# Kernel optimization log

Measured on AMD Instinct MI355X. Metric: run time of the kernel, lower is better.

## Reference

```python
import jax, jax.numpy as jnp
import numpy as np

B, C, H, W = 8, 384, 32, 32
NUM_HEADS = 8
HEAD_DIM = C // NUM_HEADS


def setup_inputs() -> dict:
    key = jax.random.key(0)
    k1, k2, k3, k4, k5 = jax.random.split(key, 5)
    s = 1.0 / np.sqrt(C)
    return {
        "x": jax.random.normal(k1, (B, C, H, W), dtype=jnp.float32),
        "w_qkv": jax.random.normal(k2, (3 * C, C), dtype=jnp.float32) * s,   # 1x1 conv == linear over channels
        "b_qkv": jax.random.normal(k3, (3 * C,), dtype=jnp.float32) * 0.01,
        "w_proj": jax.random.normal(k4, (C, C), dtype=jnp.float32) * s,
        "b_proj": jax.random.normal(k5, (C,), dtype=jnp.float32) * 0.01,
    }


def reference(x, w_qkv, b_qkv, w_proj, b_proj):
    b, c, h, w = x.shape
    n = h * w
    scale = HEAD_DIM ** (-0.5)
    # 1x1 conv qkv: (B, 3C, H, W)
    qkv = jnp.einsum('bchw,oc->bohw', x, w_qkv) + b_qkv[None, :, None, None]
    # 'b (three hd d) h0 w0 -> three b hd (h0 w0) d'
    qkv = qkv.reshape(b, 3, NUM_HEADS, HEAD_DIM, n)
    qkv = jnp.transpose(qkv, (1, 0, 2, 4, 3))  # (3, B, heads, N, d)
    q, k, v = qkv[0], qkv[1], qkv[2]
    attn = jnp.einsum('bhnd,bhmd->bhnm', q, k) * scale
    attn = jax.nn.softmax(attn, axis=-1)
    out = jnp.einsum('bhnm,bhmd->bhnd', attn, v)          # (B, heads, N, d)
    out = jnp.transpose(out, (0, 1, 3, 2)).reshape(b, c, h, w)  # b (hd d) h w
    out = jnp.einsum('bchw,oc->bohw', out, w_proj) + b_proj[None, :, None, None]
    return out
```

## Files before the change

kernel.cpp:

```cpp
#include <hip/hip_runtime.h>
#include <hip/hip_bf16.h>

typedef __hip_bfloat16 bf16;
typedef __bf16 bfx8 __attribute__((ext_vector_type(8)));
typedef float f32x4 __attribute__((ext_vector_type(4)));

#define Bk   8
#define Ck   384
#define NHk  8
#define Dk   48
#define Dp   64
#define Nk   1024
#define O3   1152


__device__ __forceinline__ void gload_lds16(const bf16* src, void* dst)
{
    __builtin_amdgcn_global_load_lds(
        (const __attribute__((address_space(1))) void*)src,
        (__attribute__((address_space(3))) void*)dst, 16, 0, 0);
}

__global__ __launch_bounds__(256) void prep_kernel(
    const float* __restrict__ x, bf16* __restrict__ Xs,
    const float* __restrict__ wq, const float* __restrict__ wp,
    bf16* __restrict__ Wq, bf16* __restrict__ Wp,
    bf16* __restrict__ Qs, bf16* __restrict__ Ks)
{
    __shared__ bf16 tile[32][33];
    if (blockIdx.x < 3072) {
        const int id = blockIdx.x;
        const int b = id / 384, rem = id % 384;
        const int c0 = ((rem >> 5) % 12) * 32, n0 = (rem & 31) * 32;
        const int tn = threadIdx.x & 31, tc = threadIdx.x >> 5;
        const float* xb = x + (size_t)b * Ck * Nk;
        #pragma unroll
        for (int i = 0; i < 4; ++i)
            tile[tc + 8 * i][tn] = __float2bfloat16(xb[(size_t)(c0 + tc + 8 * i) * Nk + n0 + tn]);
        __syncthreads();
        bf16* base = Xs + ((size_t)b * 64 + (n0 >> 4)) * 48 * 128 + (c0 >> 3) * 128;
        #pragma unroll
        for (int i = 0; i < 4; ++i) {
            int n_loc = tc + 8 * i, c_loc = tn;
            base[(size_t)(n_loc >> 4) * 6144 + (c_loc >> 3) * 128 +
                 (n_loc & 15) * 8 + (c_loc & 7)] = tile[c_loc][n_loc];
        }
    } else {
        int i = (blockIdx.x - 3072) * 256 + threadIdx.x;
        if (i < O3 * Ck) {
            int o = i / Ck, c = i - o * Ck;
            Wq[((size_t)(o >> 4) * 48 + (c >> 3)) * 128 + (o & 15) * 8 + (c & 7)] =
                __float2bfloat16(wq[i]);
        }
        if (i < Ck * Ck) {
            int o = i / Ck, c = i - o * Ck;
            Wp[((size_t)(o >> 4) * 48 + (c >> 3)) * 128 + (o & 15) * 8 + (c & 7)] =
                __float2bfloat16(wp[i]);
        }
        if (i < 262144) {
            int buf = i >> 17;
            int r17 = i & 131071;
            int head = r17 >> 11;
            int r11 = r17 & 2047;
            int g = r11 >> 5, c5 = r11 & 31;
            int cd = 6 + (c5 >> 4), e = c5 & 15;
            bf16* p = (buf ? Ks : Qs) + (size_t)head * 65536 +
                      ((size_t)g * 8 + cd) * 128 + e * 8;
            *(int4*)p = (int4){0, 0, 0, 0};
        }
    }
}

__global__ __launch_bounds__(256) void qkv_mfma_kernel(
    const bf16* __restrict__ Xs, const bf16* __restrict__ Wq,
    const float* __restrict__ bias,
    bf16* __restrict__ Qs, bf16* __restrict__ Ks, bf16* __restrict__ Vs)
{
    __shared__ __align__(16) bf16 Wl[24576];

    const int b    = blockIdx.z;
    const int by   = blockIdx.y;
    const int bx   = blockIdx.x;
    const int o0   = by * 64;
    const int n0   = bx * 128;
    const int wave = threadIdx.x >> 6;
    const int lane = threadIdx.x & 63;
    const int l15  = lane & 15, quad = lane >> 4;
    const int t3   = o0 / Ck;

    {
        const bf16* wsrc = Wq + (size_t)by * 24576;
        #pragma unroll
        for (int i = 0; i < 12; ++i) {
            int f = wave * 12 + i;
            gload_lds16(wsrc + f * 512 + lane * 8, (char*)Wl + f * 1024);
        }
    }

    const bf16* xg[2];
    #pragma unroll
    for (int i = 0; i < 2; ++i)
        xg[i] = Xs + ((size_t)(b * 64 + bx * 8 + wave * 2 + i) * 48) * 128 + lane * 8;
    const bf16* wl = Wl + lane * 8;

    f32x4 acc[8];
    #pragma unroll
    for (int i = 0; i < 8; ++i) acc[i] = (f32x4){0.f, 0.f, 0.f, 0.f};

    asm volatile("s_waitcnt vmcnt(0)" ::: "memory");
    __syncthreads();

    if (t3 < 2) {
        #pragma unroll
        for (int s = 0; s < 12; ++s) {
            bfx8 fx[2], fw[4];
            #pragma unroll
            for (int i = 0; i < 2; ++i) fx[i] = *(const bfx8*)(xg[i] + s * 512);
            #pragma unroll
            for (int j = 0; j < 4; ++j) fw[j] = *(const bfx8*)(wl + j * 6144 + s * 512);
            #pragma unroll
            for (int i = 0; i < 2; ++i)
                #pragma unroll
                for (int j = 0; j < 4; ++j)
                    acc[i * 4 + j] = __builtin_amdgcn_mfma_f32_16x16x32_bf16(
                        fx[i], fw[j], acc[i * 4 + j], 0, 0, 0);
        }
        const float qscale = 0.2082350964f;
        #pragma unroll
        for (int j = 0; j < 4; ++j) {
            int o  = o0 + j * 16 + l15;
            float bi = bias[o];
            int r  = o - t3 * Ck;
            int hd = r / Dk, d = r - hd * Dk;
            bf16* hb = (t3 == 0 ? Qs : Ks) + (size_t)(b * NHk + hd) * 65536
                     + (d >> 3) * 128 + (d & 7);
            #pragma unroll
            for (int i = 0; i < 2; ++i) {
                #pragma unroll
                for (int reg = 0; reg < 4; ++reg) {
                    int npos = n0 + wave * 32 + i * 16 + quad * 4 + reg;
                    float v = acc[i * 4 + j][reg] + bi;
                    if (t3 == 0) v *= qscale;
                    hb[(size_t)(npos >> 4) * 1024 + (npos & 15) * 8] = __float2bfloat16(v);
                }
            }
        }
    } else {
        #pragma unroll
        for (int s = 0; s < 12; ++s) {
            bfx8 fx[2], fw[4];
            #pragma unroll
            for (int i = 0; i < 2; ++i) fx[i] = *(const bfx8*)(xg[i] + s * 512);
            #pragma unroll
            for (int j = 0; j < 4; ++j) fw[j] = *(const bfx8*)(wl + j * 6144 + s * 512);
            #pragma unroll
            for (int j = 0; j < 4; ++j)
                #pragma unroll
                for (int i = 0; i < 2; ++i)
                    acc[j * 2 + i] = __builtin_amdgcn_mfma_f32_16x16x32_bf16(
                        fw[j], fx[i], acc[j * 2 + i], 0, 0, 0);
        }
        #pragma unroll
        for (int j = 0; j < 4; ++j) {
            #pragma unroll
            for (int reg = 0; reg < 4; ++reg) {
                int o  = o0 + j * 16 + quad * 4 + reg;
                float bi = bias[o];
                int r  = o - 2 * Ck;
                int hd = r / Dk, d = r - hd * Dk;
                bf16* vb = Vs + (size_t)(b * NHk + hd) * 49152
                         + ((size_t)(d >> 4) * 128) * 128 + (d & 15) * 8;
                #pragma unroll
                for (int i = 0; i < 2; ++i) {
                    int npos = n0 + wave * 32 + i * 16 + l15;
                    vb[(size_t)(npos >> 3) * 128 + (npos & 7)] =
                        __float2bfloat16(acc[j * 2 + i][reg] + bi);
                }
            }
        }
    }
}

__global__ __launch_bounds__(256, 2) void attn_kernel(
    const bf16* __restrict__ Qs, const bf16* __restrict__ Ks,
    const bf16* __restrict__ Vs, bf16* __restrict__ AO)
{
    __shared__ __align__(16) bf16 KbL[2][4096];
    __shared__ __align__(16) bf16 VbL[2][3072];
    __shared__ __align__(16) short Ps[4 * 2 * 1152];
    __shared__ float sums[4][2][16];

    const int hd   = blockIdx.x;
    const int b    = blockIdx.y;
    const int bx   = blockIdx.z;
    const int t    = threadIdx.x;
    const int wave = t >> 6;
    const int lane = t & 63;
    const int l15  = lane & 15;
    const int quad = lane >> 4;
    const int grp16 = (bx * 4 + wave) * 2;

    const bf16* qb = Qs + (size_t)(b * NHk + hd) * 65536;
    const bf16* kb = Ks + (size_t)(b * NHk + hd) * 65536;
    const bf16* vb = Vs + (size_t)(b * NHk + hd) * 49152;

    auto stage = [&](int buf, int k0) {
        const bf16* ksrc = kb + (size_t)k0 * 64;
        const bf16* vsrc = vb + (size_t)(k0 >> 3) * 128;
        char* kdst = (char*)&KbL[buf][0];
        char* vdst = (char*)&VbL[buf][0];
        #pragma unroll
        for (int i = 0; i < 4; ++i) {
            const int l = wave + i * 4;
            if (l < 14) {
                const int piece = l >> 1, half = l & 1;
                const bf16* src; char* dst;
                if (piece < 4) {
                    src = ksrc + piece * 1024 + half * 512 + lane * 8;
                    dst = kdst + piece * 2048 + half * 1024;
                } else {
                    const int dc = piece - 4;
                    src = vsrc + (size_t)dc * 16384 + half * 512 + lane * 8;
                    dst = vdst + dc * 2048 + half * 1024;
                }
                gload_lds16(src, dst);
            }
        }
    };

    stage(0, 0);

    bfx8 bq[2][2];
    #pragma unroll
    for (int qt = 0; qt < 2; ++qt) {
        const bf16* qp = qb + ((size_t)(grp16 + qt) * 8 + quad) * 128 + l15 * 8;
        bq[qt][0] = *(const bfx8*)(qp);
        bq[qt][1] = *(const bfx8*)(qp + 512);
    }

    float l_run[2] = {0.f, 0.f};
    f32x4 oacc[2][3];
    #pragma unroll
    for (int qt = 0; qt < 2; ++qt)
        #pragma unroll
        for (int dc = 0; dc < 3; ++dc) oacc[qt][dc] = (f32x4){0.f, 0.f, 0.f, 0.f};

    short* const PsW[2] = { Ps + wave * 2304, Ps + wave * 2304 + 1152 };
    const int lo = quad * 128 + l15 * 8;

    asm volatile("s_waitcnt vmcnt(0)" ::: "memory");
    __syncthreads();

    auto step = [&](int buf, int k0, bool pf) {
        if (pf) stage(buf ^ 1, k0 + 64);

        const bf16* Kc = &KbL[buf][0];
        const bf16* Vc = &VbL[buf][0];

        f32x4 sf[2][4];
        #pragma unroll
        for (int s = 0; s < 4; ++s) {
            const bfx8 kf0 = *(const bfx8*)(Kc + s * 1024 + lo);
            const bfx8 kf1 = *(const bfx8*)(Kc + s * 1024 + 512 + lo);
            #pragma unroll
            for (int qt = 0; qt < 2; ++qt) {
                f32x4 z = (f32x4){0.f, 0.f, 0.f, 0.f};
                z = __builtin_amdgcn_mfma_f32_16x16x32_bf16(kf0, bq[qt][0], z, 0, 0, 0);
                z = __builtin_amdgcn_mfma_f32_16x16x32_bf16(kf1, bq[qt][1], z, 0, 0, 0);
                sf[qt][s] = z;
            }
        }

        #pragma unroll
        for (int qt = 0; qt < 2; ++qt) {
            float lsum = 0.f;
            #pragma unroll
            for (int s = 0; s < 4; ++s) {
                ushort4 pk;
                float e0 = __builtin_amdgcn_exp2f(sf[qt][s][0]);
                float e1 = __builtin_amdgcn_exp2f(sf[qt][s][1]);
                float e2 = __builtin_amdgcn_exp2f(sf[qt][s][2]);
                float e3 = __builtin_amdgcn_exp2f(sf[qt][s][3]);
                lsum += (e0 + e1) + (e2 + e3);
                bf16 h0 = __float2bfloat16(e0), h1 = __float2bfloat16(e1);
                bf16 h2 = __float2bfloat16(e2), h3 = __float2bfloat16(e3);
                pk.x = *(unsigned short*)&h0; pk.y = *(unsigned short*)&h1;
                pk.z = *(unsigned short*)&h2; pk.w = *(unsigned short*)&h3;
                *(ushort4*)&PsW[qt][l15 * 72 + s * 16 + quad * 4] = pk;
            }
            l_run[qt] += lsum;
        }

        #pragma unroll
        for (int qt = 0; qt < 2; ++qt) {
            const bfx8 ap0 = *(const bfx8*)&PsW[qt][l15 * 72 + quad * 8];
            const bfx8 ap1 = *(const bfx8*)&PsW[qt][l15 * 72 + 32 + quad * 8];
            #pragma unroll
            for (int dc = 0; dc < 3; ++dc) {
                const bfx8 bv0 = *(const bfx8*)(Vc + dc * 1024 + lo);
                const bfx8 bv1 = *(const bfx8*)(Vc + dc * 1024 + 512 + lo);
                oacc[qt][dc] = __builtin_amdgcn_mfma_f32_16x16x32_bf16(
                    ap0, bv0, oacc[qt][dc], 0, 0, 0);
                oacc[qt][dc] = __builtin_amdgcn_mfma_f32_16x16x32_bf16(
                    ap1, bv1, oacc[qt][dc], 0, 0, 0);
            }
        }

        asm volatile("s_waitcnt vmcnt(0)" ::: "memory");
        __syncthreads();
    };

    #pragma unroll 1
    for (int k0 = 0; k0 < Nk; k0 += 128) {
        step(0, k0, true);
        step(1, k0 + 64, k0 + 128 < Nk);
    }

    #pragma unroll
    for (int qt = 0; qt < 2; ++qt) {
        float lt = l_run[qt];
        lt += __shfl_xor(lt, 16, 64);
        lt += __shfl_xor(lt, 32, 64);
        sums[wave][qt][l15] = lt;
    }

    #pragma unroll
    for (int qt = 0; qt < 2; ++qt) {
        short* OsW = PsW[qt];
        #pragma unroll
        for (int r = 0; r < 4; ++r) {
            int qi = quad * 4 + r;
            float rli = 1.0f / sums[wave][qt][qi];
            #pragma unroll
            for (int dcc = 0; dcc < 3; ++dcc) {
                bf16 hb = __float2bfloat16(oacc[qt][dcc][r] * rli);
                OsW[qi * 64 + dcc * 16 + l15] = *(short*)&hb;
            }
        }
    }

    #pragma unroll
    for (int qt = 0; qt < 2; ++qt) {
        bf16* aob = AO + (((size_t)b * 64 + grp16 + qt) * 48 + hd * 6) * 128;
        short* OsW = PsW[qt];
        int u = lane;
        int4 v = *(const int4*)&OsW[(u & 15) * 64 + (u >> 4) * 8];
        *(int4*)(aob + u * 8) = v;
        if (lane < 32) {
            int u2 = 64 + lane;
            int4 v2 = *(const int4*)&OsW[(u2 & 15) * 64 + (u2 >> 4) * 8];
            *(int4*)(aob + u2 * 8) = v2;
        }
    }
}

__global__ __launch_bounds__(256) void proj_mfma_kernel(
    const bf16* __restrict__ AO, const bf16* __restrict__ Wp,
    const float* __restrict__ bias, float* __restrict__ out)
{
    __shared__ __align__(16) bf16 Wl[24576];

    const int b    = blockIdx.z;
    const int by   = blockIdx.y;
    const int bx   = blockIdx.x;
    const int o0   = by * 64;
    const int n0   = bx * 128;
    const int wave = threadIdx.x >> 6;
    const int lane = threadIdx.x & 63;
    const int l15  = lane & 15, quad = lane >> 4;

    {
        const bf16* wsrc = Wp + (size_t)by * 24576;
        #pragma unroll
        for (int i = 0; i < 12; ++i) {
            int f = wave * 12 + i;
            gload_lds16(wsrc + f * 512 + lane * 8, (char*)Wl + f * 1024);
        }
    }

    const bf16* ag[2];
    #pragma unroll
    for (int i = 0; i < 2; ++i)
        ag[i] = AO + ((size_t)(b * 64 + bx * 8 + wave * 2 + i) * 48) * 128 + lane * 8;
    const bf16* wl = Wl + lane * 8;

    f32x4 acc[8];
    #pragma unroll
    for (int i = 0; i < 8; ++i) acc[i] = (f32x4){0.f, 0.f, 0.f, 0.f};

    asm volatile("s_waitcnt vmcnt(0)" ::: "memory");
    __syncthreads();

    #pragma unroll
    for (int s = 0; s < 12; ++s) {
        bfx8 fx[2], fw[4];
        #pragma unroll
        for (int i = 0; i < 2; ++i) fx[i] = *(const bfx8*)(ag[i] + s * 512);
        #pragma unroll
        for (int j = 0; j < 4; ++j) fw[j] = *(const bfx8*)(wl + j * 6144 + s * 512);
        #pragma unroll
        for (int j = 0; j < 4; ++j)
            #pragma unroll
            for (int i = 0; i < 2; ++i)
                acc[j * 2 + i] = __builtin_amdgcn_mfma_f32_16x16x32_bf16(
                    fw[j], fx[i], acc[j * 2 + i], 0, 0, 0);
    }

    #pragma unroll
    for (int j = 0; j < 4; ++j) {
        #pragma unroll
        for (int reg = 0; reg < 4; ++reg) {
            int o  = o0 + j * 16 + quad * 4 + reg;
            float bi = bias[o];
            #pragma unroll
            for (int i = 0; i < 2; ++i) {
                int npos = n0 + wave * 32 + i * 16 + l15;
                out[((size_t)b * Ck + o) * Nk + npos] = acc[j * 2 + i][reg] + bi;
            }
        }
    }
}

extern "C" void kernel_launch(void* const* d_in, const int* in_sizes, int n_in,
                              void* d_out, int out_size, void* d_ws, size_t ws_size,
                              hipStream_t stream)
{
    const float* x      = (const float*)d_in[0];
    const float* w_qkv  = (const float*)d_in[1];
    const float* b_qkv  = (const float*)d_in[2];
    const float* w_proj = (const float*)d_in[3];
    const float* b_proj = (const float*)d_in[4];
    float* out = (float*)d_out;

    const size_t XT_SEG = (size_t)Bk * Nk * Ck;
    const size_t WQ_SEG = (size_t)O3 * Ck;
    const size_t WP_SEG = (size_t)Ck * Ck;
    const size_t QK_SEG = (size_t)Bk * NHk * Nk * Dp;
    const size_t V_SEG  = (size_t)Bk * NHk * Dk * Nk;

    bf16* Xs = (bf16*)d_ws;
    bf16* Wq = Xs + XT_SEG;
    bf16* Wp = Wq + WQ_SEG;
    bf16* Qs = Wp + WP_SEG;
    bf16* Ks = Qs + QK_SEG;
    bf16* Vs = Ks + QK_SEG;
    bf16* AO = Vs + V_SEG;

    prep_kernel<<<3072 + (O3 * Ck + 255) / 256, 256, 0, stream>>>(
        x, Xs, w_qkv, w_proj, Wq, Wp, Qs, Ks);
    qkv_mfma_kernel<<<dim3(Nk / 128, O3 / 64, Bk), 256, 0, stream>>>(
        Xs, Wq, b_qkv, Qs, Ks, Vs);
    attn_kernel<<<dim3(NHk, Bk, 8), 256, 0, stream>>>(Qs, Ks, Vs, AO);
    proj_mfma_kernel<<<dim3(Nk / 128, Ck / 64, Bk), 256, 0, stream>>>(
        AO, Wp, b_proj, out);
}
```

Before: 120.5 us.

## Vectorize prep conversion and GEMM epilogue stores via operand swaps

The prep kernel no longer uses an LDS tile transpose. Each thread now reads 8 channel values for one position and writes a packed 16-byte bf16 chunk, and the weight conversion is packed the same way. In the QKV and projection GEMMs the MFMA operand order is swapped so each lane's accumulator registers run along the contiguous output dimension, which lets the epilogue emit 8-byte bf16 or 16-byte float stores in place of scalar ones. The attention kernel also gains explicit lgkmcnt waits and reuses a shared pack helper. The channel reads in prep are strided by N per element, so coalescing now relies on adjacent threads reading adjacent positions.

```diff
diff --git a/kernel.cpp b/kernel.cpp
--- a/kernel.cpp
+++ b/kernel.cpp
@@ -21,53 +21,68 @@
         (__attribute__((address_space(3))) void*)dst, 16, 0, 0);
 }
 
+__device__ __forceinline__ int pack2(float a, float b)
+{
+    bf16 ha = __float2bfloat16(a), hb = __float2bfloat16(b);
+    unsigned lo = *(unsigned short*)&ha, hi = *(unsigned short*)&hb;
+    return (int)(lo | (hi << 16));
+}
+
+__device__ __forceinline__ ushort4 pack4(float v0, float v1, float v2, float v3)
+{
+    bf16 h0 = __float2bfloat16(v0), h1 = __float2bfloat16(v1);
+    bf16 h2 = __float2bfloat16(v2), h3 = __float2bfloat16(v3);
+    ushort4 pk;
+    pk.x = *(unsigned short*)&h0; pk.y = *(unsigned short*)&h1;
+    pk.z = *(unsigned short*)&h2; pk.w = *(unsigned short*)&h3;
+    return pk;
+}
+
 __global__ __launch_bounds__(256) void prep_kernel(
     const float* __restrict__ x, bf16* __restrict__ Xs,
     const float* __restrict__ wq, const float* __restrict__ wp,
     bf16* __restrict__ Wq, bf16* __restrict__ Wp,
     bf16* __restrict__ Qs, bf16* __restrict__ Ks)
 {
-    __shared__ bf16 tile[32][33];
-    if (blockIdx.x < 3072) {
-        const int id = blockIdx.x;
-        const int b = id / 384, rem = id % 384;
-        const int c0 = ((rem >> 5) % 12) * 32, n0 = (rem & 31) * 32;
-        const int tn = threadIdx.x & 31, tc = threadIdx.x >> 5;
+    const int u = blockIdx.x * 256 + threadIdx.x;
+    if (u < 393216) {
+        int n = u & 1023, rest = u >> 10;
+        int oct = rest % 48, b = rest / 48;
         const float* xb = x + (size_t)b * Ck * Nk;
-        #pragma unroll
-        for (int i = 0; i < 4; ++i)
-            tile[tc + 8 * i][tn] = __float2bfloat16(xb[(size_t)(c0 + tc + 8 * i) * Nk + n0 + tn]);
-        __syncthreads();
-        bf16* base = Xs + ((size_t)b * 64 + (n0 >> 4)) * 48 * 128 + (c0 >> 3) * 128;
-        #pragma unroll
-        for (int i = 0; i < 4; ++i) {
-            int n_loc = tc + 8 * i, c_loc = tn;
-            base[(size_t)(n_loc >> 4) * 6144 + (c_loc >> 3) * 128 +
-                 (n_loc & 15) * 8 + (c_loc & 7)] = tile[c_loc][n_loc];
-        }
+        float f[8];
+        #pragma unroll
+        for (int e = 0; e < 8; ++e) f[e] = xb[(size_t)(oct * 8 + e) * Nk + n];
+        int4 v = { pack2(f[0], f[1]), pack2(f[2], f[3]),
+                   pack2(f[4], f[5]), pack2(f[6], f[7]) };
+        bf16* dst = Xs + ((size_t)b * 64 + (n >> 4)) * 6144 + oct * 128 + (n & 15) * 8;
+        *(int4*)dst = v;
+    } else if (u < 448512) {
+        int u1 = u - 393216;
+        int o = u1 % 1152, oct = u1 / 1152;
+        const float* src = wq + (size_t)o * Ck + oct * 8;
+        int4 v = { pack2(src[0], src[1]), pack2(src[2], src[3]),
+                   pack2(src[4], src[5]), pack2(src[6], src[7]) };
+        bf16* dst = Wq + ((size_t)(o >> 4) * 48 + oct) * 128 + (o & 15) * 8;
+        *(int4*)dst = v;
+    } else if (u < 466944) {
+        int u2 = u - 448512;
+        int o = u2 % 384, oct = u2 / 384;
+        const float* src = wp + (size_t)o * Ck + oct * 8;
+        int4 v = { pack2(src[0], src[1]), pack2(src[2], src[3]),
+                   pack2(src[4], src[5]), pack2(src[6], src[7]) };
+        bf16* dst = Wp + ((size_t)(o >> 4) * 48 + oct) * 128 + (o & 15) * 8;
+        *(int4*)dst = v;
     } else {
-        int i = (blockIdx.x - 3072) * 256 + threadIdx.x;
-        if (i < O3 * Ck) {
-            int o = i / Ck, c = i - o * Ck;
-            Wq[((size_t)(o >> 4) * 48 + (c >> 3)) * 128 + (o & 15) * 8 + (c & 7)] =
-                __float2bfloat16(wq[i]);
-        }
-        if (i < Ck * Ck) {
-            int o = i / Ck, c = i - o * Ck;
-            Wp[((size_t)(o >> 4) * 48 + (c >> 3)) * 128 + (o & 15) * 8 + (c & 7)] =
-                __float2bfloat16(wp[i]);
-        }
-        if (i < 262144) {
-            int buf = i >> 17;
-            int r17 = i & 131071;
-            int head = r17 >> 11;
-            int r11 = r17 & 2047;
-            int g = r11 >> 5, c5 = r11 & 31;
-            int cd = 6 + (c5 >> 4), e = c5 & 15;
-            bf16* p = (buf ? Ks : Qs) + (size_t)head * 65536 +
-                      ((size_t)g * 8 + cd) * 128 + e * 8;
-            *(int4*)p = (int4){0, 0, 0, 0};
-        }
+        int i = u - 466944;
+        int buf = i >> 17;
+        int r17 = i & 131071;
+        int head = r17 >> 11;
+        int r11 = r17 & 2047;
+        int g = r11 >> 5, c5 = r11 & 31;
+        int cd = 6 + (c5 >> 4), e = c5 & 15;
+        bf16* p = (buf ? Ks : Qs) + (size_t)head * 65536 +
+                  ((size_t)g * 8 + cd) * 128 + e * 8;
+        *(int4*)p = (int4){0, 0, 0, 0};
     }
 }
 
@@ -119,63 +134,61 @@
             #pragma unroll
             for (int j = 0; j < 4; ++j) fw[j] = *(const bfx8*)(wl + j * 6144 + s * 512);
             #pragma unroll
+            for (int j = 0; j < 4; ++j)
+                #pragma unroll
+                for (int i = 0; i < 2; ++i)
+                    acc[j * 2 + i] = __builtin_amdgcn_mfma_f32_16x16x32_bf16(
+                        fw[j], fx[i], acc[j * 2 + i], 0, 0, 0);
+        }
+        const float qscale = 0.2082350964f;
+        #pragma unroll
+        for (int j = 0; j < 4; ++j) {
+            int ob = o0 + j * 16 + quad * 4;
+            float4 bi = *(const float4*)&bias[ob];
+            int r  = ob - t3 * Ck;
+            int hd = r / Dk, d0 = r - hd * Dk;
+            bf16* hb = (t3 == 0 ? Qs : Ks) + (size_t)(b * NHk + hd) * 65536
+                     + (d0 >> 3) * 128 + (d0 & 7);
+            #pragma unroll
+            for (int i = 0; i < 2; ++i) {
+                int npos = n0 + wave * 32 + i * 16 + l15;
+                f32x4 a = acc[j * 2 + i];
+                float v0 = a[0] + bi.x, v1 = a[1] + bi.y;
+                float v2 = a[2] + bi.z, v3 = a[3] + bi.w;
+                if (t3 == 0) { v0 *= qscale; v1 *= qscale; v2 *= qscale; v3 *= qscale; }
+                *(ushort4*)(hb + (size_t)(npos >> 4) * 1024 + (npos & 15) * 8) =
+                    pack4(v0, v1, v2, v3);
+            }
+        }
+    } else {
+        #pragma unroll
+        for (int s = 0; s < 12; ++s) {
+            bfx8 fx[2], fw[4];
+            #pragma unroll
+            for (int i = 0; i < 2; ++i) fx[i] = *(const bfx8*)(xg[i] + s * 512);
+            #pragma unroll
+            for (int j = 0; j < 4; ++j) fw[j] = *(const bfx8*)(wl + j * 6144 + s * 512);
+            #pragma unroll
             for (int i = 0; i < 2; ++i)
                 #pragma unroll
                 for (int j = 0; j < 4; ++j)
                     acc[i * 4 + j] = __builtin_amdgcn_mfma_f32_16x16x32_bf16(
                         fx[i], fw[j], acc[i * 4 + j], 0, 0, 0);
         }
-        const float qscale = 0.2082350964f;
         #pragma unroll
         for (int j = 0; j < 4; ++j) {
-            int o  = o0 + j * 16 + l15;
-            float bi = bias[o];
-            int r  = o - t3 * Ck;
+            int ov = o0 + j * 16 + l15;
+            float bi = bias[ov];
+            int r  = ov - 2 * Ck;
             int hd = r / Dk, d = r - hd * Dk;
-            bf16* hb = (t3 == 0 ? Qs : Ks) + (size_t)(b * NHk + hd) * 65536
-                     + (d >> 3) * 128 + (d & 7);
+            bf16* vbp = Vs + (size_t)(b * NHk + hd) * 49152
+                      + (size_t)(d >> 4) * 16384 + (d & 15) * 8;
             #pragma unroll
             for (int i = 0; i < 2; ++i) {
-                #pragma unroll
-                for (int reg = 0; reg < 4; ++reg) {
-                    int npos = n0 + wave * 32 + i * 16 + quad * 4 + reg;
-                    float v = acc[i * 4 + j][reg] + bi;
-                    if (t3 == 0) v *= qscale;
-                    hb[(size_t)(npos >> 4) * 1024 + (npos & 15) * 8] = __float2bfloat16(v);
-                }
-            }
-        }
-    } else {
-        #pragma unroll
-        for (int s = 0; s < 12; ++s) {
-            bfx8 fx[2], fw[4];
-            #pragma unroll
-            for (int i = 0; i < 2; ++i) fx[i] = *(const bfx8*)(xg[i] + s * 512);
-            #pragma unroll
-            for (int j = 0; j < 4; ++j) fw[j] = *(const bfx8*)(wl + j * 6144 + s * 512);
-            #pragma unroll
-            for (int j = 0; j < 4; ++j)
-                #pragma unroll
-                for (int i = 0; i < 2; ++i)
-                    acc[j * 2 + i] = __builtin_amdgcn_mfma_f32_16x16x32_bf16(
-                        fw[j], fx[i], acc[j * 2 + i], 0, 0, 0);
-        }
-        #pragma unroll
-        for (int j = 0; j < 4; ++j) {
-            #pragma unroll
-            for (int reg = 0; reg < 4; ++reg) {
-                int o  = o0 + j * 16 + quad * 4 + reg;
-                float bi = bias[o];
-                int r  = o - 2 * Ck;
-                int hd = r / Dk, d = r - hd * Dk;
-                bf16* vb = Vs + (size_t)(b * NHk + hd) * 49152
-                         + ((size_t)(d >> 4) * 128) * 128 + (d & 15) * 8;
-                #pragma unroll
-                for (int i = 0; i < 2; ++i) {
-                    int npos = n0 + wave * 32 + i * 16 + l15;
-                    vb[(size_t)(npos >> 3) * 128 + (npos & 7)] =
-                        __float2bfloat16(acc[j * 2 + i][reg] + bi);
-                }
+                int npb = n0 + wave * 32 + i * 16 + quad * 4;
+                f32x4 a = acc[i * 4 + j];
+                *(ushort4*)(vbp + (size_t)(npb >> 3) * 128 + (npb & 7)) =
+                    pack4(a[0] + bi, a[1] + bi, a[2] + bi, a[3] + bi);
             }
         }
     }
@@ -276,17 +289,13 @@
             float lsum = 0.f;
             #pragma unroll
             for (int s = 0; s < 4; ++s) {
-                ushort4 pk;
                 float e0 = __builtin_amdgcn_exp2f(sf[qt][s][0]);
                 float e1 = __builtin_amdgcn_exp2f(sf[qt][s][1]);
                 float e2 = __builtin_amdgcn_exp2f(sf[qt][s][2]);
                 float e3 = __builtin_amdgcn_exp2f(sf[qt][s][3]);
                 lsum += (e0 + e1) + (e2 + e3);
-                bf16 h0 = __float2bfloat16(e0), h1 = __float2bfloat16(e1);
-                bf16 h2 = __float2bfloat16(e2), h3 = __float2bfloat16(e3);
-                pk.x = *(unsigned short*)&h0; pk.y = *(unsigned short*)&h1;
-                pk.z = *(unsigned short*)&h2; pk.w = *(unsigned short*)&h3;
-                *(ushort4*)&PsW[qt][l15 * 72 + s * 16 + quad * 4] = pk;
+                *(ushort4*)&PsW[qt][l15 * 72 + s * 16 + quad * 4] =
+                    pack4(e0, e1, e2, e3);
             }
             l_run[qt] += lsum;
         }
@@ -323,6 +332,7 @@
         lt += __shfl_xor(lt, 32, 64);
         sums[wave][qt][l15] = lt;
     }
+    asm volatile("s_waitcnt lgkmcnt(0)" ::: "memory");
 
     #pragma unroll
     for (int qt = 0; qt < 2; ++qt) {
@@ -338,6 +348,7 @@
             }
         }
     }
+    asm volatile("s_waitcnt lgkmcnt(0)" ::: "memory");
 
     #pragma unroll
     for (int qt = 0; qt < 2; ++qt) {
@@ -399,24 +410,23 @@
         #pragma unroll
         for (int j = 0; j < 4; ++j) fw[j] = *(const bfx8*)(wl + j * 6144 + s * 512);
         #pragma unroll
-        for (int j = 0; j < 4; ++j)
-            #pragma unroll
-            for (int i = 0; i < 2; ++i)
-                acc[j * 2 + i] = __builtin_amdgcn_mfma_f32_16x16x32_bf16(
-                    fw[j], fx[i], acc[j * 2 + i], 0, 0, 0);
+        for (int i = 0; i < 2; ++i)
+            #pragma unroll
+            for (int j = 0; j < 4; ++j)
+                acc[i * 4 + j] = __builtin_amdgcn_mfma_f32_16x16x32_bf16(
+                    fx[i], fw[j], acc[i * 4 + j], 0, 0, 0);
     }
 
     #pragma unroll
     for (int j = 0; j < 4; ++j) {
-        #pragma unroll
-        for (int reg = 0; reg < 4; ++reg) {
-            int o  = o0 + j * 16 + quad * 4 + reg;
-            float bi = bias[o];
-            #pragma unroll
-            for (int i = 0; i < 2; ++i) {
-                int npos = n0 + wave * 32 + i * 16 + l15;
-                out[((size_t)b * Ck + o) * Nk + npos] = acc[j * 2 + i][reg] + bi;
-            }
+        int o = o0 + j * 16 + l15;
+        float bi = bias[o];
+        #pragma unroll
+        for (int i = 0; i < 2; ++i) {
+            int npb = n0 + wave * 32 + i * 16 + quad * 4;
+            f32x4 a = acc[i * 4 + j];
+            float4 v = { a[0] + bi, a[1] + bi, a[2] + bi, a[3] + bi };
+            *(float4*)&out[((size_t)b * Ck + o) * Nk + npb] = v;
         }
     }
 }
@@ -446,8 +456,7 @@
     bf16* Vs = Ks + QK_SEG;
     bf16* AO = Vs + V_SEG;
 
-    prep_kernel<<<3072 + (O3 * Ck + 255) / 256, 256, 0, stream>>>(
-        x, Xs, w_qkv, w_proj, Wq, Wp, Qs, Ks);
+    prep_kernel<<<2848, 256, 0, stream>>>(x, Xs, w_qkv, w_proj, Wq, Wp, Qs, Ks);
     qkv_mfma_kernel<<<dim3(Nk / 128, O3 / 64, Bk), 256, 0, stream>>>(
         Xs, Wq, b_qkv, Qs, Ks, Vs);
     attn_kernel<<<dim3(NHk, Bk, 8), 256, 0, stream>>>(Qs, Ks, Vs, AO);
```

New measurement: 120.1 us. Within noise of the previous version (-0.3%).
